# Kernel optimization log

Hardware: AMD Instinct MI355X
Metric: run time of the kernel (lower is better)

Reference implementation:

```python
import jax, jax.numpy as jnp
import numpy as np

B, C, H, W = 16, 128, 128, 128
OUT, KH, KW = 256, 3, 3
PAD, STRIDE = 1, 1


def setup_inputs() -> dict:
    key = jax.random.key(0)
    k1, k2, k3, k4 = jax.random.split(key, 4)
    x = jax.random.normal(k1, (B, C, H, W), dtype=jnp.float32)
    col_kernel = jax.random.normal(k2, (C, 1, KH, 1), dtype=jnp.float32)
    row_kernel = jax.random.normal(k3, (C, 1, 1, KW), dtype=jnp.float32)
    # pointwise 1x1 conv weight, torch layout (O, C, 1, 1) -> store as (O, C)
    fan_in = C  # kaiming-uniform bound like nn.Conv2d default
    bound = float(np.sqrt(1.0 / fan_in)) * float(np.sqrt(3.0))
    pw_weight = jax.random.uniform(k4, (OUT, C), dtype=jnp.float32, minval=-bound, maxval=bound)
    return {"x": x, "col_kernel": col_kernel, "row_kernel": row_kernel, "pw_weight": pw_weight}


def reference(x, col_kernel, row_kernel, pw_weight):
    # depthwise kernel is a rank-1 outer product: (C,1,kH,1)*(C,1,1,kW) -> (C,1,kH,kW)
    dw_weight = col_kernel * row_kernel
    y = jax.lax.conv_general_dilated(
        x, dw_weight,
        window_strides=(STRIDE, STRIDE),
        padding=((PAD, PAD), (PAD, PAD)),
        dimension_numbers=("NCHW", "OIHW", "NCHW"),
        feature_group_count=C,
    )
    # pointwise 1x1 conv == channel GEMM
    out = jnp.einsum("oc,bchw->bohw", pw_weight, y)
    return out
```

## Files before the change

kernel.cpp:

```cpp
#include <hip/hip_runtime.h>

#define BB 16
#define CC 128
#define HH 128
#define WW 128
#define OO 256
#define RR 4
#define HW (HH * WW)

typedef float f32x4 __attribute__((ext_vector_type(4)));
typedef unsigned int u32x4 __attribute__((ext_vector_type(4)));
typedef short bf16x8 __attribute__((ext_vector_type(8)));

__device__ __forceinline__ unsigned short f2bf(float f) {
    unsigned int u = __float_as_uint(f);
    unsigned int r = (u + 0x7FFFu + ((u >> 16) & 1u)) >> 16;
    return (unsigned short)r;
}

__device__ __forceinline__ void gload_lds16(const void* g, void* l) {
    __builtin_amdgcn_global_load_lds(
        (const __attribute__((address_space(1))) void*)g,
        (__attribute__((address_space(3))) void*)l,
        16, 0, 0);
}

__global__ __launch_bounds__(512, 4)
void dw_rows(const float* __restrict__ x,
             const float* __restrict__ colk,
             const float* __restrict__ rowk,
             float* __restrict__ out)
{
    __shared__ __align__(16) unsigned short ybuf[WW][CC];

    const int tid  = threadIdx.x;
    const int blk  = blockIdx.x;
    const int b    = blk >> 7;
    const int hrow = blk & (HH - 1);

    const int wph = tid & 127;
    const int cg  = tid >> 7;
    const size_t base_b = (size_t)b * CC * HW;

    const bool hm  = (hrow > 0);
    const bool hp  = (hrow < HH - 1);
    const bool wmv = (wph > 0);
    const bool wpv = (wph < WW - 1);
    #pragma unroll 2
    for (int ci = 0; ci < 16; ++ci) {
        unsigned int pack = 0;
        #pragma unroll
        for (int t = 0; t < 2; ++t) {
            const int c = cg * 32 + ci * 2 + t;
            const float* xr = x + base_b + ((size_t)c * HH + hrow) * WW + wph;
            const float c0k = colk[c * 3 + 0];
            const float c1k = colk[c * 3 + 1];
            const float c2k = colk[c * 3 + 2];
            const float r0k = rowk[c * 3 + 0];
            const float r1k = rowk[c * 3 + 1];
            const float r2k = rowk[c * 3 + 2];
            float acc;
            {
                const float xm = wmv ? xr[-1] : 0.0f;
                const float xc = xr[0];
                const float xp = wpv ? xr[1] : 0.0f;
                acc = c1k * (r0k * xm + r1k * xc + r2k * xp);
            }
            if (hm) {
                const float* p = xr - WW;
                const float xm = wmv ? p[-1] : 0.0f;
                const float xc = p[0];
                const float xp = wpv ? p[1] : 0.0f;
                acc += c0k * (r0k * xm + r1k * xc + r2k * xp);
            }
            if (hp) {
                const float* p = xr + WW;
                const float xm = wmv ? p[-1] : 0.0f;
                const float xc = p[0];
                const float xp = wpv ? p[1] : 0.0f;
                acc += c2k * (r0k * xm + r1k * xc + r2k * xp);
            }
            pack |= (unsigned int)f2bf(acc) << (16 * t);
        }
        const int c = cg * 32 + ci * 2;
        const int csw = (((c >> 3) ^ (wph & 15)) << 3) | (c & 7);
        *(unsigned int*)&ybuf[wph][csw] = pack;
    }

    __syncthreads();

    float* ob = out + (size_t)b * OO * HW + (size_t)hrow * WW;
    const u32x4* src = (const u32x4*)&ybuf[0][0];
    #pragma unroll
    for (int p = 0; p < 4; ++p) {
        const int idx   = p * 512 + tid;
        const int chunk = idx >> 5;
        const int slot  = idx & 31;
        const u32x4 v = src[idx];
        *(u32x4*)((char*)(ob + (size_t)chunk * HW) + slot * 16) = v;
    }
}

__global__ __launch_bounds__(512, 2)
void pw_gemm(const float* __restrict__ pw,
             float* __restrict__ out)
{
    __shared__ __align__(16) unsigned short ybuf[2][WW][CC];

    const int tid  = threadIdx.x;
    const int lane = tid & 63;
    const int wave = tid >> 6;
    const int la   = lane & 15;
    const int qa   = lane >> 4;
    const int mg   = wave >> 1;
    const int ng   = wave & 1;

    const int blk = blockIdx.x;
    const int b   = blk >> 5;
    const int h0  = (blk & 31) * RR;

    bf16x8 afrag[4][4];
    {
        #pragma unroll
        for (int ot = 0; ot < 4; ++ot) {
            const float* prow = pw + (size_t)(mg * 64 + ot * 16 + la) * CC;
            #pragma unroll
            for (int ks = 0; ks < 4; ++ks) {
                const int c0 = ks * 32 + qa * 8;
                const float4 f0 = *(const float4*)(prow + c0);
                const float4 f1 = *(const float4*)(prow + c0 + 4);
                bf16x8 a;
                a[0] = (short)f2bf(f0.x); a[1] = (short)f2bf(f0.y);
                a[2] = (short)f2bf(f0.z); a[3] = (short)f2bf(f0.w);
                a[4] = (short)f2bf(f1.x); a[5] = (short)f2bf(f1.y);
                a[6] = (short)f2bf(f1.z); a[7] = (short)f2bf(f1.w);
                afrag[ot][ks] = a;
            }
        }
    }

    auto stage = [&](int hrow, int buf) {
        const char* gb = (const char*)(out + (size_t)b * OO * HW
                                           + (size_t)hrow * WW);
        #pragma unroll
        for (int p = 0; p < 4; ++p) {
            const int U     = p * 512 + wave * 64;
            const int idx   = U + lane;
            const int chunk = idx >> 5;
            const int slot  = idx & 31;
            const void* srcp = gb + (size_t)chunk * (HW * 4) + slot * 16;
            gload_lds16(srcp, &ybuf[buf][U >> 4][0]);
        }
    };

    auto gemm = [&](int hrow, int buf) {
        f32x4 acc[4][4];
        #pragma unroll
        for (int ot = 0; ot < 4; ++ot)
            #pragma unroll
            for (int wt = 0; wt < 4; ++wt)
                acc[ot][wt] = (f32x4){0.f, 0.f, 0.f, 0.f};

        #pragma unroll
        for (int ks = 0; ks < 4; ++ks) {
            bf16x8 bfr[4];
            const int g = ks * 4 + qa;
            #pragma unroll
            for (int wt = 0; wt < 4; ++wt) {
                const int w = ng * 64 + wt * 16 + la;
                const int csw = (g ^ la) << 3;
                bfr[wt] = *(const bf16x8*)&ybuf[buf][w][csw];
            }
            #pragma unroll
            for (int wt = 0; wt < 4; ++wt)
                #pragma unroll
                for (int ot = 0; ot < 4; ++ot)
                    acc[ot][wt] = __builtin_amdgcn_mfma_f32_16x16x32_bf16(
                        afrag[ot][ks], bfr[wt], acc[ot][wt], 0, 0, 0);
        }

        const size_t outb = (size_t)b * OO * HW + (size_t)hrow * WW;
        #pragma unroll
        for (int ot = 0; ot < 4; ++ot) {
            const int o = mg * 64 + ot * 16 + qa * 4;
            #pragma unroll
            for (int wt = 0; wt < 4; ++wt) {
                const int w = ng * 64 + wt * 16 + la;
                float* op = out + outb + (size_t)o * HW + w;
                op[0 * HW] = acc[ot][wt][0];
                op[1 * HW] = acc[ot][wt][1];
                op[2 * HW] = acc[ot][wt][2];
                op[3 * HW] = acc[ot][wt][3];
            }
        }
    };

    stage(h0, 0);
    #pragma unroll 1
    for (int r = 0; r < RR; ++r) {
        asm volatile("s_waitcnt vmcnt(0)" ::: "memory");
        __syncthreads();
        if (r + 1 < RR) stage(h0 + r + 1, (r + 1) & 1);
        gemm(h0 + r, r & 1);
    }
}

extern "C" void kernel_launch(void* const* d_in, const int* in_sizes, int n_in,
                              void* d_out, int out_size, void* d_ws, size_t ws_size,
                              hipStream_t stream) {
    const float* x    = (const float*)d_in[0];
    const float* colk = (const float*)d_in[1];
    const float* rowk = (const float*)d_in[2];
    const float* pw   = (const float*)d_in[3];
    float* out = (float*)d_out;

    hipLaunchKernelGGL(dw_rows, dim3(BB * HH), dim3(512), 0, stream,
                       x, colk, rowk, out);
    hipLaunchKernelGGL(pw_gemm, dim3(BB * (HH / RR)), dim3(512), 0, stream,
                       pw, out);
}
```

Baseline: 490.2 us.

## Vectorize depthwise loads with shuffles and transpose MFMA output for vector stores

The depthwise kernel now has each thread compute four adjacent columns from float4 loads. The horizontal neighbours come from wave shuffles instead of redundant scalar loads. The pointwise GEMM swaps the MFMA operands so each lane holds four consecutive width positions for one output channel, which allows 16-byte nontemporal stores in place of four strided scalar stores. This cuts the number of global memory instructions, but it changes the LDS write pattern, which may add bank conflicts.

```diff
diff --git a/kernel.cpp b/kernel.cpp
--- a/kernel.cpp
+++ b/kernel.cpp
@@ -38,53 +38,76 @@
     const int b    = blk >> 7;
     const int hrow = blk & (HH - 1);
 
-    const int wph = tid & 127;
-    const int cg  = tid >> 7;
+    const int wq = tid & 31;
+    const int cb = tid >> 5;
+    const int w0 = wq * 4;
     const size_t base_b = (size_t)b * CC * HW;
 
-    const bool hm  = (hrow > 0);
-    const bool hp  = (hrow < HH - 1);
-    const bool wmv = (wph > 0);
-    const bool wpv = (wph < WW - 1);
-    #pragma unroll 2
-    for (int ci = 0; ci < 16; ++ci) {
-        unsigned int pack = 0;
+    const bool hm     = (hrow > 0);
+    const bool hp     = (hrow < HH - 1);
+    const bool wfirst = (wq == 0);
+    const bool wlast  = (wq == 31);
+
+    #pragma unroll
+    for (int i = 0; i < 4; ++i) {
+        unsigned int pack[4] = {0u, 0u, 0u, 0u};
         #pragma unroll
         for (int t = 0; t < 2; ++t) {
-            const int c = cg * 32 + ci * 2 + t;
-            const float* xr = x + base_b + ((size_t)c * HH + hrow) * WW + wph;
+            const int c = cb * 8 + i * 2 + t;
+            const float* xr = x + base_b + ((size_t)c * HH + hrow) * WW + w0;
             const float c0k = colk[c * 3 + 0];
             const float c1k = colk[c * 3 + 1];
             const float c2k = colk[c * 3 + 2];
             const float r0k = rowk[c * 3 + 0];
             const float r1k = rowk[c * 3 + 1];
             const float r2k = rowk[c * 3 + 2];
-            float acc;
+            float acc0, acc1, acc2, acc3;
             {
-                const float xm = wmv ? xr[-1] : 0.0f;
-                const float xc = xr[0];
-                const float xp = wpv ? xr[1] : 0.0f;
-                acc = c1k * (r0k * xm + r1k * xc + r2k * xp);
+                const float4 v = *(const float4*)xr;
+                const float lm = __shfl_up(v.w, 1);
+                const float rn = __shfl_down(v.x, 1);
+                const float xm0 = wfirst ? 0.0f : lm;
+                const float xp3 = wlast  ? 0.0f : rn;
+                acc0 = c1k * (r0k * xm0 + r1k * v.x + r2k * v.y);
+                acc1 = c1k * (r0k * v.x + r1k * v.y + r2k * v.z);
+                acc2 = c1k * (r0k * v.y + r1k * v.z + r2k * v.w);
+                acc3 = c1k * (r0k * v.z + r1k * v.w + r2k * xp3);
             }
             if (hm) {
-                const float* p = xr - WW;
-                const float xm = wmv ? p[-1] : 0.0f;
-                const float xc = p[0];
-                const float xp = wpv ? p[1] : 0.0f;
-                acc += c0k * (r0k * xm + r1k * xc + r2k * xp);
+                const float4 v = *(const float4*)(xr - WW);
+                const float lm = __shfl_up(v.w, 1);
+                const float rn = __shfl_down(v.x, 1);
+                const float xm0 = wfirst ? 0.0f : lm;
+                const float xp3 = wlast  ? 0.0f : rn;
+                acc0 += c0k * (r0k * xm0 + r1k * v.x + r2k * v.y);
+                acc1 += c0k * (r0k * v.x + r1k * v.y + r2k * v.z);
+                acc2 += c0k * (r0k * v.y + r1k * v.z + r2k * v.w);
+                acc3 += c0k * (r0k * v.z + r1k * v.w + r2k * xp3);
             }
             if (hp) {
-                const float* p = xr + WW;
-                const float xm = wmv ? p[-1] : 0.0f;
-                const float xc = p[0];
-                const float xp = wpv ? p[1] : 0.0f;
-                acc += c2k * (r0k * xm + r1k * xc + r2k * xp);
-            }
-            pack |= (unsigned int)f2bf(acc) << (16 * t);
-        }
-        const int c = cg * 32 + ci * 2;
-        const int csw = (((c >> 3) ^ (wph & 15)) << 3) | (c & 7);
-        *(unsigned int*)&ybuf[wph][csw] = pack;
+                const float4 v = *(const float4*)(xr + WW);
+                const float lm = __shfl_up(v.w, 1);
+                const float rn = __shfl_down(v.x, 1);
+                const float xm0 = wfirst ? 0.0f : lm;
+                const float xp3 = wlast  ? 0.0f : rn;
+                acc0 += c2k * (r0k * xm0 + r1k * v.x + r2k * v.y);
+                acc1 += c2k * (r0k * v.x + r1k * v.y + r2k * v.z);
+                acc2 += c2k * (r0k * v.y + r1k * v.z + r2k * v.w);
+                acc3 += c2k * (r0k * v.z + r1k * v.w + r2k * xp3);
+            }
+            const unsigned int sh = 16 * t;
+            pack[0] |= (unsigned int)f2bf(acc0) << sh;
+            pack[1] |= (unsigned int)f2bf(acc1) << sh;
+            pack[2] |= (unsigned int)f2bf(acc2) << sh;
+            pack[3] |= (unsigned int)f2bf(acc3) << sh;
+        }
+        const int c0 = cb * 8 + i * 2;
+        #pragma unroll
+        for (int k = 0; k < 4; ++k) {
+            const int w = w0 + k;
+            const int csw = (((c0 >> 3) ^ (w & 15)) << 3) | (c0 & 7);
+            *(unsigned int*)&ybuf[w][csw] = pack[k];
+        }
     }
 
     __syncthreads();
@@ -176,21 +199,18 @@
                 #pragma unroll
                 for (int ot = 0; ot < 4; ++ot)
                     acc[ot][wt] = __builtin_amdgcn_mfma_f32_16x16x32_bf16(
-                        afrag[ot][ks], bfr[wt], acc[ot][wt], 0, 0, 0);
+                        bfr[wt], afrag[ot][ks], acc[ot][wt], 0, 0, 0);
         }
 
         const size_t outb = (size_t)b * OO * HW + (size_t)hrow * WW;
         #pragma unroll
         for (int ot = 0; ot < 4; ++ot) {
-            const int o = mg * 64 + ot * 16 + qa * 4;
+            const int o = mg * 64 + ot * 16 + la;
             #pragma unroll
             for (int wt = 0; wt < 4; ++wt) {
-                const int w = ng * 64 + wt * 16 + la;
+                const int w = ng * 64 + wt * 16 + qa * 4;
                 float* op = out + outb + (size_t)o * HW + w;
-                op[0 * HW] = acc[ot][wt][0];
-                op[1 * HW] = acc[ot][wt][1];
-                op[2 * HW] = acc[ot][wt][2];
-                op[3 * HW] = acc[ot][wt][3];
+                __builtin_nontemporal_store(acc[ot][wt], (f32x4*)op);
             }
         }
     };
```

New measurement: 430.8 us. -12.1%, faster.
